# Kernel tuning notes

Measured on AMD Instinct MI355X. Metric: run time of the kernel, lower is better.

The kernel has to match this reference:

```python
import jax, jax.numpy as jnp
import numpy as np

N_NODES = 500_000
N_EDGES = 16_000_000
GCN_DIMS = [1, 4, 7, 10, 16]   # gcn layer in/out widths
MLP_DIMS = [16, 32, 16, 16]    # fc1, fc2, fc3 (raw_feature_size=16)


def setup_inputs() -> dict:
    key = jax.random.key(0)
    ks = list(jax.random.split(key, 40))
    ki = iter(ks)
    inp = {}
    inp["x"] = jax.random.normal(next(ki), (N_NODES, 1), dtype=jnp.float32)
    inp["edge_index"] = jax.random.randint(next(ki), (2, N_EDGES), 0, N_NODES, dtype=jnp.int32)
    # GraphConv params: lin_rel (weight+bias) applied to aggregated neighbors,
    # lin_root (weight, no bias) applied to self features.
    for li in range(4):
        din, dout = GCN_DIMS[li], GCN_DIMS[li + 1]
        s = 1.0 / np.sqrt(din)
        inp[f"g{li+1}_Wrel"] = jax.random.uniform(next(ki), (din, dout), jnp.float32, -s, s)
        inp[f"g{li+1}_brel"] = jax.random.uniform(next(ki), (dout,), jnp.float32, -s, s)
        inp[f"g{li+1}_Wroot"] = jax.random.uniform(next(ki), (din, dout), jnp.float32, -s, s)
    for li in range(3):
        din, dout = MLP_DIMS[li], MLP_DIMS[li + 1]
        s = 1.0 / np.sqrt(din)
        inp[f"fc{li+1}_W"] = jax.random.uniform(next(ki), (din, dout), jnp.float32, -s, s)
        inp[f"fc{li+1}_b"] = jax.random.uniform(next(ki), (dout,), jnp.float32, -s, s)
    return inp


def _graph_conv(x, Wrel, brel, Wroot, src, dst):
    # PyG GraphConv, aggr='add': out_i = Wrel @ (sum_{j->i} x_j) + brel + Wroot @ x_i
    agg = jax.ops.segment_sum(x[src], dst, num_segments=N_NODES)  # [N, din]
    return agg @ Wrel + brel + x @ Wroot


def reference(x, edge_index,
              g1_Wrel, g1_brel, g1_Wroot,
              g2_Wrel, g2_brel, g2_Wroot,
              g3_Wrel, g3_brel, g3_Wroot,
              g4_Wrel, g4_brel, g4_Wroot,
              fc1_W, fc1_b, fc2_W, fc2_b, fc3_W, fc3_b):
    src, dst = edge_index[0], edge_index[1]
    h = jax.nn.relu(_graph_conv(x, g1_Wrel, g1_brel, g1_Wroot, src, dst))
    h = jax.nn.relu(_graph_conv(h, g2_Wrel, g2_brel, g2_Wroot, src, dst))
    h = jax.nn.relu(_graph_conv(h, g3_Wrel, g3_brel, g3_Wroot, src, dst))
    h = jax.nn.relu(_graph_conv(h, g4_Wrel, g4_brel, g4_Wroot, src, dst))
    h = jax.nn.relu(h @ fc1_W + fc1_b)
    h = jax.nn.relu(h @ fc2_W + fc2_b)
    return h @ fc3_W + fc3_b
```

## Files before the change

kernel.cpp:

```cpp
#include <hip/hip_runtime.h>
#include <hip/hip_fp16.h>

#define N_NODES 500000
#define N_EDGES 16000000

#define SB_BITS 13
#define SB_SIZE (1 << SB_BITS)
#define NSUPER ((N_NODES + SB_SIZE - 1) / SB_SIZE)
#define CAP1 270336
#define BKT_BITS 9
#define BKT_SIZE (1 << BKT_BITS)
#define NBUCKET ((N_NODES + BKT_SIZE - 1) / BKT_SIZE)
#define BKT_CAP 18432
#define B1_EPT 256
#define B1_CHUNK (256 * B1_EPT)
#define B1_NBLK ((N_EDGES + B1_CHUNK - 1) / B1_CHUNK)
#define B1_VQ (B1_EPT / 4)
#define NV4 (N_EDGES / 4)
#define B2_PER_SUPER 8

typedef unsigned int u32x2 __attribute__((ext_vector_type(2)));
typedef unsigned int u32x4 __attribute__((ext_vector_type(4)));
typedef float f32x2 __attribute__((ext_vector_type(2)));
typedef float f32x4 __attribute__((ext_vector_type(4)));

__device__ __forceinline__ unsigned int h2u(__half2 h) { return *(unsigned int*)&h; }

__global__ __launch_bounds__(512) void init_bcur_kernel(
    int* __restrict__ bcur1, int* __restrict__ bcur2)
{
    int i = blockIdx.x * 512 + threadIdx.x;
    if (i < NSUPER) bcur1[i] = i * CAP1;
    if (i < NBUCKET) bcur2[i] = i * BKT_CAP;
}

__global__ __launch_bounds__(256) void bin1_kernel(
    const int* __restrict__ src, const int* __restrict__ dst,
    int* __restrict__ bcur1, unsigned int* __restrict__ pairs1)
{
    __shared__ int lh[NSUPER];
    __shared__ int lbase[NSUPER];
    const int4* dst4 = (const int4*)dst;
    const int4* src4 = (const int4*)src;
    int t = threadIdx.x;
    long v0 = (long)blockIdx.x * (B1_CHUNK / 4);

    if (t < NSUPER) lh[t] = 0;
    __syncthreads();

#pragma unroll 8
    for (int q = 0; q < B1_VQ; ++q) {
        long v = v0 + q * 256 + t;
        if (v < NV4) {
            int4 d = dst4[v];
            atomicAdd(&lh[d.x >> SB_BITS], 1);
            atomicAdd(&lh[d.y >> SB_BITS], 1);
            atomicAdd(&lh[d.z >> SB_BITS], 1);
            atomicAdd(&lh[d.w >> SB_BITS], 1);
        }
    }
    __syncthreads();

    if (t < NSUPER) {
        int c = lh[t];
        lbase[t] = c ? atomicAdd(&bcur1[t], c) : 0;
        lh[t] = 0;
    }
    __syncthreads();

#pragma unroll 8
    for (int q = 0; q < B1_VQ; ++q) {
        long v = v0 + q * 256 + t;
        if (v < NV4) {
            int4 d = dst4[v];
            int4 s = src4[v];
            {
                int b = d.x >> SB_BITS;
                int r = atomicAdd(&lh[b], 1);
                pairs1[lbase[b] + r] = ((unsigned int)s.x << SB_BITS) | (unsigned int)(d.x & (SB_SIZE - 1));
            }
            {
                int b = d.y >> SB_BITS;
                int r = atomicAdd(&lh[b], 1);
                pairs1[lbase[b] + r] = ((unsigned int)s.y << SB_BITS) | (unsigned int)(d.y & (SB_SIZE - 1));
            }
            {
                int b = d.z >> SB_BITS;
                int r = atomicAdd(&lh[b], 1);
                pairs1[lbase[b] + r] = ((unsigned int)s.z << SB_BITS) | (unsigned int)(d.z & (SB_SIZE - 1));
            }
            {
                int b = d.w >> SB_BITS;
                int r = atomicAdd(&lh[b], 1);
                pairs1[lbase[b] + r] = ((unsigned int)s.w << SB_BITS) | (unsigned int)(d.w & (SB_SIZE - 1));
            }
        }
    }
}

__global__ __launch_bounds__(256) void bin2_kernel(
    const int* __restrict__ bcur1, int* __restrict__ bcur2,
    const unsigned int* __restrict__ pairs1, unsigned int* __restrict__ pairs2)
{
    __shared__ int lh[16];
    __shared__ int lbase[16];
    int s = blockIdx.x >> 3;
    int blk = blockIdx.x & 7;
    int t = threadIdx.x;
    int count = bcur1[s] - s * CAP1;
    int chunk = (((count + B2_PER_SUPER - 1) / B2_PER_SUPER) + 3) & ~3;
    int lo = blk * chunk;
    int hi = lo + chunk; if (hi > count) hi = count;
    int len = hi > lo ? hi - lo : 0;
    const unsigned int* base = pairs1 + (size_t)s * CAP1 + lo;
    const uint4* p4 = (const uint4*)base;
    int nv = len >> 2;

    if (t < 16) lh[t] = 0;
    __syncthreads();

    for (int i = t; i < nv; i += 256) {
        uint4 p = p4[i];
        atomicAdd(&lh[(p.x & (SB_SIZE - 1)) >> BKT_BITS], 1);
        atomicAdd(&lh[(p.y & (SB_SIZE - 1)) >> BKT_BITS], 1);
        atomicAdd(&lh[(p.z & (SB_SIZE - 1)) >> BKT_BITS], 1);
        atomicAdd(&lh[(p.w & (SB_SIZE - 1)) >> BKT_BITS], 1);
    }
    if (t < (len & 3))
        atomicAdd(&lh[(base[(nv << 2) + t] & (SB_SIZE - 1)) >> BKT_BITS], 1);
    __syncthreads();

    if (t < 16) {
        int c = lh[t];
        lbase[t] = c ? atomicAdd(&bcur2[(s << 4) | t], c) : 0;
        lh[t] = 0;
    }
    __syncthreads();

    for (int i = t; i < nv; i += 256) {
        uint4 p = p4[i];
#pragma unroll
        for (int q = 0; q < 4; ++q) {
            unsigned int e = (q == 0) ? p.x : (q == 1) ? p.y : (q == 2) ? p.z : p.w;
            int sub = (int)((e & (SB_SIZE - 1)) >> BKT_BITS);
            int r = atomicAdd(&lh[sub], 1);
            pairs2[lbase[sub] + r] = ((e >> SB_BITS) << BKT_BITS) | (e & (BKT_SIZE - 1));
        }
    }
    if (t < (len & 3)) {
        unsigned int e = base[(nv << 2) + t];
        int sub = (int)((e & (SB_SIZE - 1)) >> BKT_BITS);
        int r = atomicAdd(&lh[sub], 1);
        pairs2[lbase[sub] + r] = ((e >> SB_BITS) << BKT_BITS) | (e & (BKT_SIZE - 1));
    }
}

__global__ __launch_bounds__(512) void bucket_scan_kernel(
    const int* __restrict__ bcur2, int* __restrict__ bbase)
{
    __shared__ int sdata[512];
    int t = threadIdx.x;
    int i0 = t * 2;
    int v0 = (i0 < NBUCKET) ? (bcur2[i0] - i0 * BKT_CAP) : 0;
    int v1 = (i0 + 1 < NBUCKET) ? (bcur2[i0 + 1] - (i0 + 1) * BKT_CAP) : 0;
    int s = v0 + v1;
    sdata[t] = s;
    __syncthreads();
    for (int o = 1; o < 512; o <<= 1) {
        int tmp = (t >= o) ? sdata[t - o] : 0;
        __syncthreads();
        sdata[t] += tmp;
        __syncthreads();
    }
    int run = sdata[t] - s;
    if (i0 < NBUCKET) bbase[i0] = run;
    if (i0 + 1 < NBUCKET) bbase[i0 + 1] = run + v0;
    if (i0 == NBUCKET - 1) bbase[NBUCKET] = run + v0;
    if (i0 + 1 == NBUCKET - 1) bbase[NBUCKET] = run + v0 + v1;
}

__global__ __launch_bounds__(512) void bucket_sort512_kernel(
    const int* __restrict__ bcur2, const int* __restrict__ bbase,
    const unsigned int* __restrict__ pairs2, const float* __restrict__ xfeat,
    int* __restrict__ off, int* __restrict__ sorted_src,
    float* __restrict__ agg1)
{
    __shared__ int   stage[BKT_CAP];
    __shared__ int   lh[BKT_SIZE];
    __shared__ float laccum[BKT_SIZE];
    __shared__ int   sdata[512];
    int b = blockIdx.x;
    int t = threadIdx.x;
    int base_node = b << BKT_BITS;
    size_t pstart = (size_t)b * BKT_CAP;
    int count = bcur2[b] - b * BKT_CAP;
    int cstart = bbase[b];

    lh[t] = 0; laccum[t] = 0.0f;
    __syncthreads();

    int nv = count >> 2;
    const uint4* p4 = (const uint4*)(pairs2 + pstart);
    for (int i = t; i < nv; i += 512) {
        uint4 p = p4[i];
        atomicAdd(&lh[p.x & (BKT_SIZE - 1)], 1);
        atomicAdd(&lh[p.y & (BKT_SIZE - 1)], 1);
        atomicAdd(&lh[p.z & (BKT_SIZE - 1)], 1);
        atomicAdd(&lh[p.w & (BKT_SIZE - 1)], 1);
    }
    if (t < (count & 3))
        atomicAdd(&lh[pairs2[pstart + (nv << 2) + t] & (BKT_SIZE - 1)], 1);
    __syncthreads();

    int c = lh[t];
    sdata[t] = c;
    __syncthreads();
    for (int o = 1; o < 512; o <<= 1) {
        int tmp = (t >= o) ? sdata[t - o] : 0;
        __syncthreads();
        sdata[t] += tmp;
        __syncthreads();
    }
    int run = cstart + sdata[t] - c;
    int node = base_node + t;
    if (node < N_NODES) {
        off[node] = run;
        if (node == N_NODES - 1) off[N_NODES] = run + c;
    }
    lh[t] = run;
    __syncthreads();

    for (int i = t; i < nv; i += 512) {
        uint4 p = p4[i];
#pragma unroll
        for (int q = 0; q < 4; ++q) {
            unsigned int pe = (q == 0) ? p.x : (q == 1) ? p.y : (q == 2) ? p.z : p.w;
            int low = (int)(pe & (BKT_SIZE - 1));
            int sidx = (int)(pe >> BKT_BITS);
            int pos = atomicAdd(&lh[low], 1);
            stage[pos - cstart] = sidx;
            atomicAdd(&laccum[low], xfeat[sidx]);
        }
    }
    if (t < (count & 3)) {
        unsigned int pe = pairs2[pstart + (nv << 2) + t];
        int low = (int)(pe & (BKT_SIZE - 1));
        int sidx = (int)(pe >> BKT_BITS);
        int pos = atomicAdd(&lh[low], 1);
        stage[pos - cstart] = sidx;
        atomicAdd(&laccum[low], xfeat[sidx]);
    }
    __syncthreads();

    for (int j = t; j < count; j += 512)
        __builtin_nontemporal_store(stage[j], &sorted_src[cstart + j]);
    if (node < N_NODES) __builtin_nontemporal_store(laccum[t], &agg1[node]);
}

__global__ __launch_bounds__(256) void transform1_kernel(
    const float* __restrict__ agg1, const float* __restrict__ x,
    const float* __restrict__ Wrel, const float* __restrict__ brel,
    const float* __restrict__ Wroot,
    __half2* __restrict__ h1)
{
    __shared__ float w[12];
    if (threadIdx.x < 4) {
        w[threadIdx.x] = Wrel[threadIdx.x];
        w[4 + threadIdx.x] = brel[threadIdx.x];
        w[8 + threadIdx.x] = Wroot[threadIdx.x];
    }
    __syncthreads();
    int i = blockIdx.x * blockDim.x + threadIdx.x;
    if (i >= N_NODES) return;
    float a = agg1[i], xv = x[i];
    float r0 = fmaxf(a * w[0] + w[4] + xv * w[8],  0.0f);
    float r1 = fmaxf(a * w[1] + w[5] + xv * w[9],  0.0f);
    float r2 = fmaxf(a * w[2] + w[6] + xv * w[10], 0.0f);
    float r3 = fmaxf(a * w[3] + w[7] + xv * w[11], 0.0f);
    u32x2 v = { h2u(__floats2half2_rn(r0, r1)), h2u(__floats2half2_rn(r2, r3)) };
    __builtin_nontemporal_store(v, (u32x2*)(h1 + (size_t)i * 2));
}

__global__ __launch_bounds__(256) void gather2t_kernel(
    const int* __restrict__ off, const int* __restrict__ ss,
    const __half2* __restrict__ h1,
    const float* __restrict__ Wrel, const float* __restrict__ brel,
    const float* __restrict__ Wroot,
    __half2* __restrict__ h2)
{
    __shared__ float tile[128 * 5];
    __shared__ float sWr[28], sWo[28], sb[7];
    int t = threadIdx.x;
    if (t < 28) { sWr[t] = Wrel[t]; sWo[t] = Wroot[t]; }
    if (t < 7) sb[t] = brel[t];

    int ln = t >> 1;
    int j = t & 1;
    int node = blockIdx.x * 128 + ln;
    if (node < N_NODES) {
        int start = off[node], end = off[node + 1];
        float a0x=0,a0y=0,a1x=0,a1y=0,a2x=0,a2y=0,a3x=0,a3y=0;
        float b0x=0,b0y=0,b1x=0,b1y=0,b2x=0,b2y=0,b3x=0,b3y=0;
        int e = start;
        for (; e + 8 <= end; e += 8) {
            int s0=ss[e],s1=ss[e+1],s2=ss[e+2],s3=ss[e+3];
            int s4=ss[e+4],s5=ss[e+5],s6=ss[e+6],s7=ss[e+7];
            float2 f0=__half22float2(h1[(size_t)s0*2+j]);
            float2 f1=__half22float2(h1[(size_t)s1*2+j]);
            float2 f2=__half22float2(h1[(size_t)s2*2+j]);
            float2 f3=__half22float2(h1[(size_t)s3*2+j]);
            float2 f4=__half22float2(h1[(size_t)s4*2+j]);
            float2 f5=__half22float2(h1[(size_t)s5*2+j]);
            float2 f6=__half22float2(h1[(size_t)s6*2+j]);
            float2 f7=__half22float2(h1[(size_t)s7*2+j]);
            a0x+=f0.x;a0y+=f0.y; a1x+=f1.x;a1y+=f1.y;
            a2x+=f2.x;a2y+=f2.y; a3x+=f3.x;a3y+=f3.y;
            b0x+=f4.x;b0y+=f4.y; b1x+=f5.x;b1y+=f5.y;
            b2x+=f6.x;b2y+=f6.y; b3x+=f7.x;b3y+=f7.y;
        }
        for (; e < end; ++e) {
            float2 f = __half22float2(h1[(size_t)ss[e]*2+j]);
            a0x += f.x; a0y += f.y;
        }
        float rx = ((a0x+a1x)+(a2x+a3x)) + ((b0x+b1x)+(b2x+b3x));
        float ry = ((a0y+a1y)+(a2y+a3y)) + ((b0y+b1y)+(b2y+b3y));
        tile[ln * 5 + 2 * j] = rx;
        tile[ln * 5 + 2 * j + 1] = ry;
    }
    __syncthreads();

    if (t < 128) {
        int n2 = blockIdx.x * 128 + t;
        if (n2 < N_NODES) {
            float av[4];
#pragma unroll
            for (int k = 0; k < 4; ++k) av[k] = tile[t * 5 + k];
            float2 x01 = __half22float2(h1[(size_t)n2 * 2]);
            float2 x23 = __half22float2(h1[(size_t)n2 * 2 + 1]);
            float xv[4] = {x01.x, x01.y, x23.x, x23.y};
            float o_[8];
#pragma unroll
            for (int o = 0; o < 7; ++o) {
                float v = sb[o];
#pragma unroll
                for (int k = 0; k < 4; ++k)
                    v += av[k] * sWr[k * 7 + o] + xv[k] * sWo[k * 7 + o];
                o_[o] = fmaxf(v, 0.0f);
            }
            o_[7] = 0.0f;
            u32x4 v = { h2u(__floats2half2_rn(o_[0], o_[1])),
                        h2u(__floats2half2_rn(o_[2], o_[3])),
                        h2u(__floats2half2_rn(o_[4], o_[5])),
                        h2u(__floats2half2_rn(o_[6], o_[7])) };
            __builtin_nontemporal_store(v, (u32x4*)(h2 + (size_t)n2 * 4));
        }
    }
}

__global__ __launch_bounds__(256) void gather3t_kernel(
    const int* __restrict__ off, const int* __restrict__ ss,
    const __half2* __restrict__ h2,
    const float* __restrict__ Wrel, const float* __restrict__ brel,
    const float* __restrict__ Wroot,
    __half2* __restrict__ h3)
{
    __shared__ float tile[64 * 9];
    __shared__ float sWr[70], sWo[70], sb[10];
    int t = threadIdx.x;
    if (t < 70) { sWr[t] = Wrel[t]; sWo[t] = Wroot[t]; }
    if (t < 10) sb[t] = brel[t];

    int ln = t >> 2;
    int j = t & 3;
    int node = blockIdx.x * 64 + ln;
    if (node < N_NODES) {
        int start = off[node], end = off[node + 1];
        float a0x=0,a0y=0,a1x=0,a1y=0,a2x=0,a2y=0,a3x=0,a3y=0;
        float b0x=0,b0y=0,b1x=0,b1y=0,b2x=0,b2y=0,b3x=0,b3y=0;
        int e = start;
        for (; e + 8 <= end; e += 8) {
            int s0=ss[e],s1=ss[e+1],s2=ss[e+2],s3=ss[e+3];
            int s4=ss[e+4],s5=ss[e+5],s6=ss[e+6],s7=ss[e+7];
            float2 f0=__half22float2(h2[(size_t)s0*4+j]);
            float2 f1=__half22float2(h2[(size_t)s1*4+j]);
            float2 f2=__half22float2(h2[(size_t)s2*4+j]);
            float2 f3=__half22float2(h2[(size_t)s3*4+j]);
            float2 f4=__half22float2(h2[(size_t)s4*4+j]);
            float2 f5=__half22float2(h2[(size_t)s5*4+j]);
            float2 f6=__half22float2(h2[(size_t)s6*4+j]);
            float2 f7=__half22float2(h2[(size_t)s7*4+j]);
            a0x+=f0.x;a0y+=f0.y; a1x+=f1.x;a1y+=f1.y;
            a2x+=f2.x;a2y+=f2.y; a3x+=f3.x;a3y+=f3.y;
            b0x+=f4.x;b0y+=f4.y; b1x+=f5.x;b1y+=f5.y;
            b2x+=f6.x;b2y+=f6.y; b3x+=f7.x;b3y+=f7.y;
        }
        for (; e < end; ++e) {
            float2 f = __half22float2(h2[(size_t)ss[e]*4+j]);
            a0x += f.x; a0y += f.y;
        }
        float rx = ((a0x+a1x)+(a2x+a3x)) + ((b0x+b1x)+(b2x+b3x));
        float ry = ((a0y+a1y)+(a2y+a3y)) + ((b0y+b1y)+(b2y+b3y));
        tile[ln * 9 + 2 * j] = rx;
        tile[ln * 9 + 2 * j + 1] = ry;
    }
    __syncthreads();

    if (t < 64) {
        int n2 = blockIdx.x * 64 + t;
        if (n2 < N_NODES) {
            float av[7];
#pragma unroll
            for (int k = 0; k < 7; ++k) av[k] = tile[t * 9 + k];
            float xv[8];
#pragma unroll
            for (int q = 0; q < 4; ++q) {
                float2 f = __half22float2(h2[(size_t)n2 * 4 + q]);
                xv[2 * q] = f.x; xv[2 * q + 1] = f.y;
            }
            float o_[16];
#pragma unroll
            for (int o = 0; o < 10; ++o) {
                float v = sb[o];
#pragma unroll
                for (int k = 0; k < 7; ++k)
                    v += av[k] * sWr[k * 10 + o] + xv[k] * sWo[k * 10 + o];
                o_[o] = fmaxf(v, 0.0f);
            }
#pragma unroll
            for (int o = 10; o < 16; ++o) o_[o] = 0.0f;
            u32x4 v0 = { h2u(__floats2half2_rn(o_[0], o_[1])),
                         h2u(__floats2half2_rn(o_[2], o_[3])),
                         h2u(__floats2half2_rn(o_[4], o_[5])),
                         h2u(__floats2half2_rn(o_[6], o_[7])) };
            u32x4 v1 = { h2u(__floats2half2_rn(o_[8], o_[9])),
                         h2u(__floats2half2_rn(o_[10], o_[11])),
                         h2u(__floats2half2_rn(o_[12], o_[13])),
                         h2u(__floats2half2_rn(o_[14], o_[15])) };
            __builtin_nontemporal_store(v0, (u32x4*)(h3 + (size_t)n2 * 8));
            __builtin_nontemporal_store(v1, (u32x4*)(h3 + (size_t)n2 * 8 + 4));
        }
    }
}

__global__ __launch_bounds__(256) void gather4_kernel(
    const int* __restrict__ off, const int* __restrict__ ss,
    const __half2* __restrict__ h3, float* __restrict__ agg)
{
    int node = blockIdx.x * 32 + (threadIdx.x >> 3);
    int j = threadIdx.x & 7;
    if (node >= N_NODES) return;
    int start = off[node], end = off[node + 1];

    float a0x=0,a0y=0,a1x=0,a1y=0,a2x=0,a2y=0,a3x=0,a3y=0;
    float b0x=0,b0y=0,b1x=0,b1y=0,b2x=0,b2y=0,b3x=0,b3y=0;
    int e = start;
    for (; e + 8 <= end; e += 8) {
        int s0=ss[e],s1=ss[e+1],s2=ss[e+2],s3=ss[e+3];
        int s4=ss[e+4],s5=ss[e+5],s6=ss[e+6],s7=ss[e+7];
        float2 f0=__half22float2(h3[(size_t)s0*8+j]);
        float2 f1=__half22float2(h3[(size_t)s1*8+j]);
        float2 f2=__half22float2(h3[(size_t)s2*8+j]);
        float2 f3=__half22float2(h3[(size_t)s3*8+j]);
        float2 f4=__half22float2(h3[(size_t)s4*8+j]);
        float2 f5=__half22float2(h3[(size_t)s5*8+j]);
        float2 f6=__half22float2(h3[(size_t)s6*8+j]);
        float2 f7=__half22float2(h3[(size_t)s7*8+j]);
        a0x+=f0.x;a0y+=f0.y; a1x+=f1.x;a1y+=f1.y;
        a2x+=f2.x;a2y+=f2.y; a3x+=f3.x;a3y+=f3.y;
        b0x+=f4.x;b0y+=f4.y; b1x+=f5.x;b1y+=f5.y;
        b2x+=f6.x;b2y+=f6.y; b3x+=f7.x;b3y+=f7.y;
    }
    for (; e < end; ++e) {
        float2 f = __half22float2(h3[(size_t)ss[e]*8+j]);
        a0x += f.x; a0y += f.y;
    }
    float rx = ((a0x+a1x)+(a2x+a3x)) + ((b0x+b1x)+(b2x+b3x));
    float ry = ((a0y+a1y)+(a2y+a3y)) + ((b0y+b1y)+(b2y+b3y));
    f32x2 v = { rx, ry };
    __builtin_nontemporal_store(v, (f32x2*)(agg + (size_t)node * 16 + j * 2));
}

__global__ __launch_bounds__(256) void layer4_mlp_kernel(
    const float* __restrict__ agg, const __half2* __restrict__ h3,
    const float* __restrict__ g4Wrel, const float* __restrict__ g4brel,
    const float* __restrict__ g4Wroot,
    const float* __restrict__ fc1W, const float* __restrict__ fc1b,
    const float* __restrict__ fc2W, const float* __restrict__ fc2b,
    const float* __restrict__ fc3W, const float* __restrict__ fc3b,
    float* __restrict__ out)
{
    __shared__ float s[1680];
    float* sWrel  = s;
    float* sbrel  = s + 160;
    float* sWroot = s + 176;
    float* sfc1W  = s + 336;
    float* sfc1b  = s + 848;
    float* sfc2W  = s + 880;
    float* sfc2b  = s + 1392;
    float* sfc3W  = s + 1408;
    float* sfc3b  = s + 1664;
    int t = threadIdx.x;
    for (int i = t; i < 160; i += 256) { sWrel[i] = g4Wrel[i]; sWroot[i] = g4Wroot[i]; }
    for (int i = t; i < 512; i += 256) { sfc1W[i] = fc1W[i]; sfc2W[i] = fc2W[i]; }
    if (t < 256) sfc3W[t] = fc3W[t];
    if (t < 32)  sfc1b[t] = fc1b[t];
    if (t < 16)  { sbrel[t] = g4brel[t]; sfc2b[t] = fc2b[t]; sfc3b[t] = fc3b[t]; }
    __syncthreads();

    int i = blockIdx.x * blockDim.x + threadIdx.x;
    if (i >= N_NODES) return;

    const float4* ap = (const float4*)(agg + (size_t)i * 16);
    float4 a0 = ap[0], a1 = ap[1], a2 = ap[2];
    float a[10] = {a0.x, a0.y, a0.z, a0.w, a1.x, a1.y, a1.z, a1.w, a2.x, a2.y};
    float xin[10];
#pragma unroll
    for (int q = 0; q < 5; ++q) {
        float2 f = __half22float2(h3[(size_t)i * 8 + q]);
        xin[2 * q] = f.x; xin[2 * q + 1] = f.y;
    }

    float h4[16];
#pragma unroll
    for (int o = 0; o < 16; ++o) {
        float v = sbrel[o];
#pragma unroll
        for (int k = 0; k < 10; ++k)
            v += a[k] * sWrel[k * 16 + o] + xin[k] * sWroot[k * 16 + o];
        h4[o] = fmaxf(v, 0.0f);
    }
    float m1[32];
#pragma unroll
    for (int o = 0; o < 32; ++o) {
        float v = sfc1b[o];
#pragma unroll
        for (int k = 0; k < 16; ++k) v += h4[k] * sfc1W[k * 32 + o];
        m1[o] = fmaxf(v, 0.0f);
    }
    float m2[16];
#pragma unroll
    for (int o = 0; o < 16; ++o) {
        float v = sfc2b[o];
#pragma unroll
        for (int k = 0; k < 32; ++k) v += m1[k] * sfc2W[k * 16 + o];
        m2[o] = fmaxf(v, 0.0f);
    }
    float r[16];
#pragma unroll
    for (int o = 0; o < 16; ++o) {
        float v = sfc3b[o];
#pragma unroll
        for (int k = 0; k < 16; ++k) v += m2[k] * sfc3W[k * 16 + o];
        r[o] = v;
    }
#pragma unroll
    for (int q = 0; q < 4; ++q) {
        f32x4 v = { r[q*4+0], r[q*4+1], r[q*4+2], r[q*4+3] };
        __builtin_nontemporal_store(v, (f32x4*)(out + (size_t)i * 16 + q * 4));
    }
}

extern "C" void kernel_launch(void* const* d_in, const int* in_sizes, int n_in,
                              void* d_out, int out_size, void* d_ws, size_t ws_size,
                              hipStream_t stream) {
    const float* x        = (const float*)d_in[0];
    const int*   ei       = (const int*)d_in[1];
    const float* g1_Wrel  = (const float*)d_in[2];
    const float* g1_brel  = (const float*)d_in[3];
    const float* g1_Wroot = (const float*)d_in[4];
    const float* g2_Wrel  = (const float*)d_in[5];
    const float* g2_brel  = (const float*)d_in[6];
    const float* g2_Wroot = (const float*)d_in[7];
    const float* g3_Wrel  = (const float*)d_in[8];
    const float* g3_brel  = (const float*)d_in[9];
    const float* g3_Wroot = (const float*)d_in[10];
    const float* g4_Wrel  = (const float*)d_in[11];
    const float* g4_brel  = (const float*)d_in[12];
    const float* g4_Wroot = (const float*)d_in[13];
    const float* fc1_W    = (const float*)d_in[14];
    const float* fc1_b    = (const float*)d_in[15];
    const float* fc2_W    = (const float*)d_in[16];
    const float* fc2_b    = (const float*)d_in[17];
    const float* fc3_W    = (const float*)d_in[18];
    const float* fc3_b    = (const float*)d_in[19];
    float* out = (float*)d_out;

    const int* srcp = ei;
    const int* dstp = ei + N_EDGES;

    char* p = (char*)d_ws;
    auto alloc = [&](size_t bytes) {
        char* r = p;
        p += (bytes + 255) & ~(size_t)255;
        return r;
    };
    __half2* h1  = (__half2*)alloc((size_t)N_NODES * 4 * 2);
    __half2* h2  = (__half2*)alloc((size_t)N_NODES * 8 * 2);
    __half2* h3  = (__half2*)alloc((size_t)N_NODES * 16 * 2);
    float*   agg = (float*)  alloc((size_t)N_NODES * 16 * 4);
    alloc((size_t)14 * 1024 * 1024);
    unsigned int* pairs2 = (unsigned int*)h1;
    int* sorted_src = (int*)alloc((size_t)NSUPER * CAP1 * 4);
    unsigned int* pairs1 = (unsigned int*)sorted_src;
    int*   off   = (int*)alloc((size_t)(N_NODES + 1) * 4);
    float* agg1  = (float*)alloc((size_t)N_NODES * 4);
    int*   bcur1 = (int*)alloc((size_t)NSUPER * 4);
    int*   bcur2 = (int*)alloc((size_t)NBUCKET * 4);
    int*   bbase = (int*)alloc((size_t)(NBUCKET + 1) * 4);

    const int TB = 256;
    const int node_blocks = (N_NODES + TB - 1) / TB;

    init_bcur_kernel<<<2, 512, 0, stream>>>(bcur1, bcur2);
    bin1_kernel<<<B1_NBLK, 256, 0, stream>>>(srcp, dstp, bcur1, pairs1);
    bin2_kernel<<<NSUPER * B2_PER_SUPER, 256, 0, stream>>>(bcur1, bcur2, pairs1, pairs2);
    bucket_scan_kernel<<<1, 512, 0, stream>>>(bcur2, bbase);
    bucket_sort512_kernel<<<NBUCKET, 512, 0, stream>>>(
        bcur2, bbase, pairs2, x, off, sorted_src, agg1);

    transform1_kernel<<<node_blocks, TB, 0, stream>>>(
        agg1, x, g1_Wrel, g1_brel, g1_Wroot, h1);

    gather2t_kernel<<<(N_NODES + 127) / 128, TB, 0, stream>>>(
        off, sorted_src, h1, g2_Wrel, g2_brel, g2_Wroot, h2);
    gather3t_kernel<<<(N_NODES + 63) / 64, TB, 0, stream>>>(
        off, sorted_src, h2, g3_Wrel, g3_brel, g3_Wroot, h3);

    gather4_kernel<<<(N_NODES + 31) / 32, TB, 0, stream>>>(off, sorted_src, h3, agg);
    layer4_mlp_kernel<<<node_blocks, TB, 0, stream>>>(
        agg, h3, g4_Wrel, g4_brel, g4_Wroot,
        fc1_W, fc1_b, fc2_W, fc2_b, fc3_W, fc3_b, out);
}
```

Before: 882.3 us.

## Switch gather kernels to one thread per node with vectorized row loads

The layer 2-4 gather kernels now assign one thread to each destination node instead of splitting a node's feature row across 2, 4 or 8 threads. Each thread loads the whole fp16 neighbor row as a single uint2/uint4 (or two uint4) and does the dense transform itself, so the shared-memory tile and the second phase after __syncthreads go away. This cuts redundant index loads and issues wider memory transactions. In exchange, lanes within a wavefront diverge more on degree, load coalescing across lanes drops, and register pressure rises from the 16 accumulators.

After: 993.4 us. 1.13x slower.

```diff
diff --git a/kernel.cpp b/kernel.cpp
--- a/kernel.cpp
+++ b/kernel.cpp
@@ -21,10 +21,10 @@
 
 typedef unsigned int u32x2 __attribute__((ext_vector_type(2)));
 typedef unsigned int u32x4 __attribute__((ext_vector_type(4)));
-typedef float f32x2 __attribute__((ext_vector_type(2)));
 typedef float f32x4 __attribute__((ext_vector_type(4)));
 
 __device__ __forceinline__ unsigned int h2u(__half2 h) { return *(unsigned int*)&h; }
+__device__ __forceinline__ float2 u2f2(unsigned int u) { return __half22float2(*(__half2*)&u); }
 
 __global__ __launch_bounds__(512) void init_bcur_kernel(
     int* __restrict__ bcur1, int* __restrict__ bcur2)
@@ -288,73 +288,57 @@
     const float* __restrict__ Wroot,
     __half2* __restrict__ h2)
 {
-    __shared__ float tile[128 * 5];
     __shared__ float sWr[28], sWo[28], sb[7];
     int t = threadIdx.x;
     if (t < 28) { sWr[t] = Wrel[t]; sWo[t] = Wroot[t]; }
     if (t < 7) sb[t] = brel[t];
-
-    int ln = t >> 1;
-    int j = t & 1;
-    int node = blockIdx.x * 128 + ln;
-    if (node < N_NODES) {
-        int start = off[node], end = off[node + 1];
-        float a0x=0,a0y=0,a1x=0,a1y=0,a2x=0,a2y=0,a3x=0,a3y=0;
-        float b0x=0,b0y=0,b1x=0,b1y=0,b2x=0,b2y=0,b3x=0,b3y=0;
-        int e = start;
-        for (; e + 8 <= end; e += 8) {
-            int s0=ss[e],s1=ss[e+1],s2=ss[e+2],s3=ss[e+3];
-            int s4=ss[e+4],s5=ss[e+5],s6=ss[e+6],s7=ss[e+7];
-            float2 f0=__half22float2(h1[(size_t)s0*2+j]);
-            float2 f1=__half22float2(h1[(size_t)s1*2+j]);
-            float2 f2=__half22float2(h1[(size_t)s2*2+j]);
-            float2 f3=__half22float2(h1[(size_t)s3*2+j]);
-            float2 f4=__half22float2(h1[(size_t)s4*2+j]);
-            float2 f5=__half22float2(h1[(size_t)s5*2+j]);
-            float2 f6=__half22float2(h1[(size_t)s6*2+j]);
-            float2 f7=__half22float2(h1[(size_t)s7*2+j]);
-            a0x+=f0.x;a0y+=f0.y; a1x+=f1.x;a1y+=f1.y;
-            a2x+=f2.x;a2y+=f2.y; a3x+=f3.x;a3y+=f3.y;
-            b0x+=f4.x;b0y+=f4.y; b1x+=f5.x;b1y+=f5.y;
-            b2x+=f6.x;b2y+=f6.y; b3x+=f7.x;b3y+=f7.y;
-        }
-        for (; e < end; ++e) {
-            float2 f = __half22float2(h1[(size_t)ss[e]*2+j]);
-            a0x += f.x; a0y += f.y;
-        }
-        float rx = ((a0x+a1x)+(a2x+a3x)) + ((b0x+b1x)+(b2x+b3x));
-        float ry = ((a0y+a1y)+(a2y+a3y)) + ((b0y+b1y)+(b2y+b3y));
-        tile[ln * 5 + 2 * j] = rx;
-        tile[ln * 5 + 2 * j + 1] = ry;
-    }
-    __syncthreads();
-
-    if (t < 128) {
-        int n2 = blockIdx.x * 128 + t;
-        if (n2 < N_NODES) {
-            float av[4];
-#pragma unroll
-            for (int k = 0; k < 4; ++k) av[k] = tile[t * 5 + k];
-            float2 x01 = __half22float2(h1[(size_t)n2 * 2]);
-            float2 x23 = __half22float2(h1[(size_t)n2 * 2 + 1]);
-            float xv[4] = {x01.x, x01.y, x23.x, x23.y};
-            float o_[8];
-#pragma unroll
-            for (int o = 0; o < 7; ++o) {
-                float v = sb[o];
-#pragma unroll
-                for (int k = 0; k < 4; ++k)
-                    v += av[k] * sWr[k * 7 + o] + xv[k] * sWo[k * 7 + o];
-                o_[o] = fmaxf(v, 0.0f);
-            }
-            o_[7] = 0.0f;
-            u32x4 v = { h2u(__floats2half2_rn(o_[0], o_[1])),
-                        h2u(__floats2half2_rn(o_[2], o_[3])),
-                        h2u(__floats2half2_rn(o_[4], o_[5])),
-                        h2u(__floats2half2_rn(o_[6], o_[7])) };
-            __builtin_nontemporal_store(v, (u32x4*)(h2 + (size_t)n2 * 4));
-        }
-    }
+    __syncthreads();
+
+    int node = blockIdx.x * 256 + t;
+    if (node >= N_NODES) return;
+    int start = off[node], end = off[node + 1];
+    const uint2* hv = (const uint2*)h1;
+
+    float a0=0,a1=0,a2=0,a3=0, c0=0,c1=0,c2=0,c3=0;
+    int e = start;
+    for (; e + 8 <= end; e += 8) {
+        uint2 u0 = hv[ss[e+0]], u1 = hv[ss[e+1]], u2 = hv[ss[e+2]], u3 = hv[ss[e+3]];
+        uint2 u4 = hv[ss[e+4]], u5 = hv[ss[e+5]], u6 = hv[ss[e+6]], u7 = hv[ss[e+7]];
+        float2 f;
+        f = u2f2(u0.x); a0+=f.x; a1+=f.y;  f = u2f2(u0.y); a2+=f.x; a3+=f.y;
+        f = u2f2(u1.x); c0+=f.x; c1+=f.y;  f = u2f2(u1.y); c2+=f.x; c3+=f.y;
+        f = u2f2(u2.x); a0+=f.x; a1+=f.y;  f = u2f2(u2.y); a2+=f.x; a3+=f.y;
+        f = u2f2(u3.x); c0+=f.x; c1+=f.y;  f = u2f2(u3.y); c2+=f.x; c3+=f.y;
+        f = u2f2(u4.x); a0+=f.x; a1+=f.y;  f = u2f2(u4.y); a2+=f.x; a3+=f.y;
+        f = u2f2(u5.x); c0+=f.x; c1+=f.y;  f = u2f2(u5.y); c2+=f.x; c3+=f.y;
+        f = u2f2(u6.x); a0+=f.x; a1+=f.y;  f = u2f2(u6.y); a2+=f.x; a3+=f.y;
+        f = u2f2(u7.x); c0+=f.x; c1+=f.y;  f = u2f2(u7.y); c2+=f.x; c3+=f.y;
+    }
+    for (; e < end; ++e) {
+        uint2 u = hv[ss[e]];
+        float2 f;
+        f = u2f2(u.x); a0+=f.x; a1+=f.y;  f = u2f2(u.y); a2+=f.x; a3+=f.y;
+    }
+    float av[4] = {a0+c0, a1+c1, a2+c2, a3+c3};
+
+    float2 x01 = __half22float2(h1[(size_t)node * 2]);
+    float2 x23 = __half22float2(h1[(size_t)node * 2 + 1]);
+    float xv[4] = {x01.x, x01.y, x23.x, x23.y};
+    float o_[8];
+#pragma unroll
+    for (int o = 0; o < 7; ++o) {
+        float v = sb[o];
+#pragma unroll
+        for (int k = 0; k < 4; ++k)
+            v += av[k] * sWr[k * 7 + o] + xv[k] * sWo[k * 7 + o];
+        o_[o] = fmaxf(v, 0.0f);
+    }
+    o_[7] = 0.0f;
+    u32x4 v = { h2u(__floats2half2_rn(o_[0], o_[1])),
+                h2u(__floats2half2_rn(o_[2], o_[3])),
+                h2u(__floats2half2_rn(o_[4], o_[5])),
+                h2u(__floats2half2_rn(o_[6], o_[7])) };
+    __builtin_nontemporal_store(v, (u32x4*)(h2 + (size_t)node * 4));
 }
 
 __global__ __launch_bounds__(256) void gather3t_kernel(
@@ -364,120 +348,125 @@
     const float* __restrict__ Wroot,
     __half2* __restrict__ h3)
 {
-    __shared__ float tile[64 * 9];
     __shared__ float sWr[70], sWo[70], sb[10];
     int t = threadIdx.x;
     if (t < 70) { sWr[t] = Wrel[t]; sWo[t] = Wroot[t]; }
     if (t < 10) sb[t] = brel[t];
-
-    int ln = t >> 2;
-    int j = t & 3;
-    int node = blockIdx.x * 64 + ln;
-    if (node < N_NODES) {
-        int start = off[node], end = off[node + 1];
-        float a0x=0,a0y=0,a1x=0,a1y=0,a2x=0,a2y=0,a3x=0,a3y=0;
-        float b0x=0,b0y=0,b1x=0,b1y=0,b2x=0,b2y=0,b3x=0,b3y=0;
-        int e = start;
-        for (; e + 8 <= end; e += 8) {
-            int s0=ss[e],s1=ss[e+1],s2=ss[e+2],s3=ss[e+3];
-            int s4=ss[e+4],s5=ss[e+5],s6=ss[e+6],s7=ss[e+7];
-            float2 f0=__half22float2(h2[(size_t)s0*4+j]);
-            float2 f1=__half22float2(h2[(size_t)s1*4+j]);
-            float2 f2=__half22float2(h2[(size_t)s2*4+j]);
-            float2 f3=__half22float2(h2[(size_t)s3*4+j]);
-            float2 f4=__half22float2(h2[(size_t)s4*4+j]);
-            float2 f5=__half22float2(h2[(size_t)s5*4+j]);
-            float2 f6=__half22float2(h2[(size_t)s6*4+j]);
-            float2 f7=__half22float2(h2[(size_t)s7*4+j]);
-            a0x+=f0.x;a0y+=f0.y; a1x+=f1.x;a1y+=f1.y;
-            a2x+=f2.x;a2y+=f2.y; a3x+=f3.x;a3y+=f3.y;
-            b0x+=f4.x;b0y+=f4.y; b1x+=f5.x;b1y+=f5.y;
-            b2x+=f6.x;b2y+=f6.y; b3x+=f7.x;b3y+=f7.y;
-        }
-        for (; e < end; ++e) {
-            float2 f = __half22float2(h2[(size_t)ss[e]*4+j]);
-            a0x += f.x; a0y += f.y;
-        }
-        float rx = ((a0x+a1x)+(a2x+a3x)) + ((b0x+b1x)+(b2x+b3x));
-        float ry = ((a0y+a1y)+(a2y+a3y)) + ((b0y+b1y)+(b2y+b3y));
-        tile[ln * 9 + 2 * j] = rx;
-        tile[ln * 9 + 2 * j + 1] = ry;
-    }
-    __syncthreads();
-
-    if (t < 64) {
-        int n2 = blockIdx.x * 64 + t;
-        if (n2 < N_NODES) {
-            float av[7];
-#pragma unroll
-            for (int k = 0; k < 7; ++k) av[k] = tile[t * 9 + k];
-            float xv[8];
-#pragma unroll
-            for (int q = 0; q < 4; ++q) {
-                float2 f = __half22float2(h2[(size_t)n2 * 4 + q]);
-                xv[2 * q] = f.x; xv[2 * q + 1] = f.y;
-            }
-            float o_[16];
-#pragma unroll
-            for (int o = 0; o < 10; ++o) {
-                float v = sb[o];
-#pragma unroll
-                for (int k = 0; k < 7; ++k)
-                    v += av[k] * sWr[k * 10 + o] + xv[k] * sWo[k * 10 + o];
-                o_[o] = fmaxf(v, 0.0f);
-            }
-#pragma unroll
-            for (int o = 10; o < 16; ++o) o_[o] = 0.0f;
-            u32x4 v0 = { h2u(__floats2half2_rn(o_[0], o_[1])),
-                         h2u(__floats2half2_rn(o_[2], o_[3])),
-                         h2u(__floats2half2_rn(o_[4], o_[5])),
-                         h2u(__floats2half2_rn(o_[6], o_[7])) };
-            u32x4 v1 = { h2u(__floats2half2_rn(o_[8], o_[9])),
-                         h2u(__floats2half2_rn(o_[10], o_[11])),
-                         h2u(__floats2half2_rn(o_[12], o_[13])),
-                         h2u(__floats2half2_rn(o_[14], o_[15])) };
-            __builtin_nontemporal_store(v0, (u32x4*)(h3 + (size_t)n2 * 8));
-            __builtin_nontemporal_store(v1, (u32x4*)(h3 + (size_t)n2 * 8 + 4));
-        }
-    }
+    __syncthreads();
+
+    int node = blockIdx.x * 256 + t;
+    if (node >= N_NODES) return;
+    int start = off[node], end = off[node + 1];
+    const uint4* hv = (const uint4*)h2;
+
+    float a[8] = {0,0,0,0,0,0,0,0};
+    float c[8] = {0,0,0,0,0,0,0,0};
+    int e = start;
+    for (; e + 8 <= end; e += 8) {
+        uint4 u0 = hv[ss[e+0]], u1 = hv[ss[e+1]], u2 = hv[ss[e+2]], u3 = hv[ss[e+3]];
+        uint4 u4 = hv[ss[e+4]], u5 = hv[ss[e+5]], u6 = hv[ss[e+6]], u7 = hv[ss[e+7]];
+        float2 f;
+        f=u2f2(u0.x); a[0]+=f.x;a[1]+=f.y; f=u2f2(u0.y); a[2]+=f.x;a[3]+=f.y;
+        f=u2f2(u0.z); a[4]+=f.x;a[5]+=f.y; f=u2f2(u0.w); a[6]+=f.x;a[7]+=f.y;
+        f=u2f2(u1.x); c[0]+=f.x;c[1]+=f.y; f=u2f2(u1.y); c[2]+=f.x;c[3]+=f.y;
+        f=u2f2(u1.z); c[4]+=f.x;c[5]+=f.y; f=u2f2(u1.w); c[6]+=f.x;c[7]+=f.y;
+        f=u2f2(u2.x); a[0]+=f.x;a[1]+=f.y; f=u2f2(u2.y); a[2]+=f.x;a[3]+=f.y;
+        f=u2f2(u2.z); a[4]+=f.x;a[5]+=f.y; f=u2f2(u2.w); a[6]+=f.x;a[7]+=f.y;
+        f=u2f2(u3.x); c[0]+=f.x;c[1]+=f.y; f=u2f2(u3.y); c[2]+=f.x;c[3]+=f.y;
+        f=u2f2(u3.z); c[4]+=f.x;c[5]+=f.y; f=u2f2(u3.w); c[6]+=f.x;c[7]+=f.y;
+        f=u2f2(u4.x); a[0]+=f.x;a[1]+=f.y; f=u2f2(u4.y); a[2]+=f.x;a[3]+=f.y;
+        f=u2f2(u4.z); a[4]+=f.x;a[5]+=f.y; f=u2f2(u4.w); a[6]+=f.x;a[7]+=f.y;
+        f=u2f2(u5.x); c[0]+=f.x;c[1]+=f.y; f=u2f2(u5.y); c[2]+=f.x;c[3]+=f.y;
+        f=u2f2(u5.z); c[4]+=f.x;c[5]+=f.y; f=u2f2(u5.w); c[6]+=f.x;c[7]+=f.y;
+        f=u2f2(u6.x); a[0]+=f.x;a[1]+=f.y; f=u2f2(u6.y); a[2]+=f.x;a[3]+=f.y;
+        f=u2f2(u6.z); a[4]+=f.x;a[5]+=f.y; f=u2f2(u6.w); a[6]+=f.x;a[7]+=f.y;
+        f=u2f2(u7.x); c[0]+=f.x;c[1]+=f.y; f=u2f2(u7.y); c[2]+=f.x;c[3]+=f.y;
+        f=u2f2(u7.z); c[4]+=f.x;c[5]+=f.y; f=u2f2(u7.w); c[6]+=f.x;c[7]+=f.y;
+    }
+    for (; e < end; ++e) {
+        uint4 u = hv[ss[e]];
+        float2 f;
+        f=u2f2(u.x); a[0]+=f.x;a[1]+=f.y; f=u2f2(u.y); a[2]+=f.x;a[3]+=f.y;
+        f=u2f2(u.z); a[4]+=f.x;a[5]+=f.y; f=u2f2(u.w); a[6]+=f.x;a[7]+=f.y;
+    }
+    float av[7];
+#pragma unroll
+    for (int k = 0; k < 7; ++k) av[k] = a[k] + c[k];
+
+    float xv[8];
+#pragma unroll
+    for (int q = 0; q < 4; ++q) {
+        float2 f = __half22float2(h2[(size_t)node * 4 + q]);
+        xv[2 * q] = f.x; xv[2 * q + 1] = f.y;
+    }
+    float o_[16];
+#pragma unroll
+    for (int o = 0; o < 10; ++o) {
+        float v = sb[o];
+#pragma unroll
+        for (int k = 0; k < 7; ++k)
+            v += av[k] * sWr[k * 10 + o] + xv[k] * sWo[k * 10 + o];
+        o_[o] = fmaxf(v, 0.0f);
+    }
+#pragma unroll
+    for (int o = 10; o < 16; ++o) o_[o] = 0.0f;
+    u32x4 v0 = { h2u(__floats2half2_rn(o_[0], o_[1])),
+                 h2u(__floats2half2_rn(o_[2], o_[3])),
+                 h2u(__floats2half2_rn(o_[4], o_[5])),
+                 h2u(__floats2half2_rn(o_[6], o_[7])) };
+    u32x4 v1 = { h2u(__floats2half2_rn(o_[8], o_[9])),
+                 h2u(__floats2half2_rn(o_[10], o_[11])),
+                 h2u(__floats2half2_rn(o_[12], o_[13])),
+                 h2u(__floats2half2_rn(o_[14], o_[15])) };
+    __builtin_nontemporal_store(v0, (u32x4*)(h3 + (size_t)node * 8));
+    __builtin_nontemporal_store(v1, (u32x4*)(h3 + (size_t)node * 8 + 4));
 }
 
 __global__ __launch_bounds__(256) void gather4_kernel(
     const int* __restrict__ off, const int* __restrict__ ss,
     const __half2* __restrict__ h3, float* __restrict__ agg)
 {
-    int node = blockIdx.x * 32 + (threadIdx.x >> 3);
-    int j = threadIdx.x & 7;
+    int node = blockIdx.x * 256 + threadIdx.x;
     if (node >= N_NODES) return;
     int start = off[node], end = off[node + 1];
-
-    float a0x=0,a0y=0,a1x=0,a1y=0,a2x=0,a2y=0,a3x=0,a3y=0;
-    float b0x=0,b0y=0,b1x=0,b1y=0,b2x=0,b2y=0,b3x=0,b3y=0;
+    const uint4* hv = (const uint4*)h3;
+
+    float a[16] = {0,0,0,0,0,0,0,0,0,0,0,0,0,0,0,0};
     int e = start;
-    for (; e + 8 <= end; e += 8) {
-        int s0=ss[e],s1=ss[e+1],s2=ss[e+2],s3=ss[e+3];
-        int s4=ss[e+4],s5=ss[e+5],s6=ss[e+6],s7=ss[e+7];
-        float2 f0=__half22float2(h3[(size_t)s0*8+j]);
-        float2 f1=__half22float2(h3[(size_t)s1*8+j]);
-        float2 f2=__half22float2(h3[(size_t)s2*8+j]);
-        float2 f3=__half22float2(h3[(size_t)s3*8+j]);
-        float2 f4=__half22float2(h3[(size_t)s4*8+j]);
-        float2 f5=__half22float2(h3[(size_t)s5*8+j]);
-        float2 f6=__half22float2(h3[(size_t)s6*8+j]);
-        float2 f7=__half22float2(h3[(size_t)s7*8+j]);
-        a0x+=f0.x;a0y+=f0.y; a1x+=f1.x;a1y+=f1.y;
-        a2x+=f2.x;a2y+=f2.y; a3x+=f3.x;a3y+=f3.y;
-        b0x+=f4.x;b0y+=f4.y; b1x+=f5.x;b1y+=f5.y;
-        b2x+=f6.x;b2y+=f6.y; b3x+=f7.x;b3y+=f7.y;
+    for (; e + 4 <= end; e += 4) {
+        int s0 = ss[e+0], s1 = ss[e+1], s2 = ss[e+2], s3 = ss[e+3];
+        uint4 u0a = hv[(size_t)s0*2], u0b = hv[(size_t)s0*2+1];
+        uint4 u1a = hv[(size_t)s1*2], u1b = hv[(size_t)s1*2+1];
+        uint4 u2a = hv[(size_t)s2*2], u2b = hv[(size_t)s2*2+1];
+        uint4 u3a = hv[(size_t)s3*2], u3b = hv[(size_t)s3*2+1];
+        float2 f;
+        f=u2f2(u0a.x); a[0]+=f.x;a[1]+=f.y; f=u2f2(u0a.y); a[2]+=f.x;a[3]+=f.y;
+        f=u2f2(u0a.z); a[4]+=f.x;a[5]+=f.y; f=u2f2(u0a.w); a[6]+=f.x;a[7]+=f.y;
+        f=u2f2(u0b.x); a[8]+=f.x;a[9]+=f.y; f=u2f2(u0b.y); a[10]+=f.x;a[11]+=f.y;
+        f=u2f2(u1a.x); a[0]+=f.x;a[1]+=f.y; f=u2f2(u1a.y); a[2]+=f.x;a[3]+=f.y;
+        f=u2f2(u1a.z); a[4]+=f.x;a[5]+=f.y; f=u2f2(u1a.w); a[6]+=f.x;a[7]+=f.y;
+        f=u2f2(u1b.x); a[8]+=f.x;a[9]+=f.y; f=u2f2(u1b.y); a[10]+=f.x;a[11]+=f.y;
+        f=u2f2(u2a.x); a[0]+=f.x;a[1]+=f.y; f=u2f2(u2a.y); a[2]+=f.x;a[3]+=f.y;
+        f=u2f2(u2a.z); a[4]+=f.x;a[5]+=f.y; f=u2f2(u2a.w); a[6]+=f.x;a[7]+=f.y;
+        f=u2f2(u2b.x); a[8]+=f.x;a[9]+=f.y; f=u2f2(u2b.y); a[10]+=f.x;a[11]+=f.y;
+        f=u2f2(u3a.x); a[0]+=f.x;a[1]+=f.y; f=u2f2(u3a.y); a[2]+=f.x;a[3]+=f.y;
+        f=u2f2(u3a.z); a[4]+=f.x;a[5]+=f.y; f=u2f2(u3a.w); a[6]+=f.x;a[7]+=f.y;
+        f=u2f2(u3b.x); a[8]+=f.x;a[9]+=f.y; f=u2f2(u3b.y); a[10]+=f.x;a[11]+=f.y;
     }
     for (; e < end; ++e) {
-        float2 f = __half22float2(h3[(size_t)ss[e]*8+j]);
-        a0x += f.x; a0y += f.y;
-    }
-    float rx = ((a0x+a1x)+(a2x+a3x)) + ((b0x+b1x)+(b2x+b3x));
-    float ry = ((a0y+a1y)+(a2y+a3y)) + ((b0y+b1y)+(b2y+b3y));
-    f32x2 v = { rx, ry };
-    __builtin_nontemporal_store(v, (f32x2*)(agg + (size_t)node * 16 + j * 2));
+        int s0 = ss[e];
+        uint4 ua = hv[(size_t)s0*2], ub = hv[(size_t)s0*2+1];
+        float2 f;
+        f=u2f2(ua.x); a[0]+=f.x;a[1]+=f.y; f=u2f2(ua.y); a[2]+=f.x;a[3]+=f.y;
+        f=u2f2(ua.z); a[4]+=f.x;a[5]+=f.y; f=u2f2(ua.w); a[6]+=f.x;a[7]+=f.y;
+        f=u2f2(ub.x); a[8]+=f.x;a[9]+=f.y; f=u2f2(ub.y); a[10]+=f.x;a[11]+=f.y;
+    }
+    a[12] = a[13] = a[14] = a[15] = 0.0f;
+#pragma unroll
+    for (int q = 0; q < 4; ++q) {
+        f32x4 v = { a[q*4+0], a[q*4+1], a[q*4+2], a[q*4+3] };
+        __builtin_nontemporal_store(v, (f32x4*)(agg + (size_t)node * 16 + q * 4));
+    }
 }
 
 __global__ __launch_bounds__(256) void layer4_mlp_kernel(
@@ -621,12 +610,12 @@
     transform1_kernel<<<node_blocks, TB, 0, stream>>>(
         agg1, x, g1_Wrel, g1_brel, g1_Wroot, h1);
 
-    gather2t_kernel<<<(N_NODES + 127) / 128, TB, 0, stream>>>(
+    gather2t_kernel<<<node_blocks, TB, 0, stream>>>(
         off, sorted_src, h1, g2_Wrel, g2_brel, g2_Wroot, h2);
-    gather3t_kernel<<<(N_NODES + 63) / 64, TB, 0, stream>>>(
+    gather3t_kernel<<<node_blocks, TB, 0, stream>>>(
         off, sorted_src, h2, g3_Wrel, g3_brel, g3_Wroot, h3);
 
-    gather4_kernel<<<(N_NODES + 31) / 32, TB, 0, stream>>>(off, sorted_src, h3, agg);
+    gather4_kernel<<<node_blocks, TB, 0, stream>>>(off, sorted_src, h3, agg);
     layer4_mlp_kernel<<<node_blocks, TB, 0, stream>>>(
         agg, h3, g4_Wrel, g4_brel, g4_Wroot,
         fc1_W, fc1_b, fc2_W, fc2_b, fc3_W, fc3_b, out);
```
